# Optimization experiments

Hardware: AMD Instinct MI355X
Metric: run time of the kernel (lower is better)

## Reference

```python
import jax, jax.numpy as jnp
import numpy as np

CH = 512      # channels
CI = CH // 4  # in_channel = 128
DILS = (1, 4, 8, 12)
GN_GROUPS = 32


def conv2d(x, w, dil=1, pad=0):
    # x: (N,Cin,H,W), w: (Cout,Cin,kh,kw)
    return jax.lax.conv_general_dilated(
        x, w, window_strides=(1, 1), padding=[(pad, pad), (pad, pad)],
        rhs_dilation=(dil, dil),
        dimension_numbers=('NCHW', 'OIHW', 'NCHW'))


def group_norm(x, gamma, beta, groups=GN_GROUPS, eps=1e-5):
    N, C, H, W = x.shape
    xg = x.reshape(N, groups, C // groups, H, W)
    mu = jnp.mean(xg, axis=(2, 3, 4), keepdims=True)
    var = jnp.var(xg, axis=(2, 3, 4), keepdims=True)
    xn = ((xg - mu) * jax.lax.rsqrt(var + eps)).reshape(N, C, H, W)
    return xn * gamma[None, :, None, None] + beta[None, :, None, None]


def dyn_branch(xd, w_cat, d):
    # dynamic filter: (N, 9, H, W), softmax over the K=9 taps per pixel
    f = jax.nn.softmax(conv2d(xd, w_cat, dil=d, pad=d), axis=1)
    N, C, H, W = xd.shape
    xp = jnp.pad(xd, ((0, 0), (0, 0), (d, d), (d, d)))
    # fused unfold + weighted sum: accumulate 9 shifted views * per-pixel weight
    out = jnp.zeros_like(xd)
    k = 0
    for i in range(3):
        for j in range(3):
            out = out + xp[:, :, i * d:i * d + H, j * d:j * d + W] * f[:, k:k + 1]
            k += 1
    return out


def setup_inputs():
    key = jax.random.key(0)
    ks = jax.random.split(key, 16)
    s = 0.05
    return {
        'x': jax.random.normal(ks[0], (4, CH, 128, 128), jnp.float32),
        'w_scale1': jax.random.normal(ks[1], (CI, CH, 1, 1), jnp.float32) * s,
        'gn1_g': jnp.ones((CI,), jnp.float32),
        'gn1_b': jnp.zeros((CI,), jnp.float32),
        'w_cata': jax.random.normal(ks[2], (9, CI, 3, 3), jnp.float32) * s,
        'w_catb': jax.random.normal(ks[3], (9, CI, 3, 3), jnp.float32) * s,
        'w_catc': jax.random.normal(ks[4], (9, CI, 3, 3), jnp.float32) * s,
        'w_catd': jax.random.normal(ks[5], (9, CI, 3, 3), jnp.float32) * s,
        'w_scale2': jax.random.normal(ks[6], (CI, 5 * CI, 1, 1), jnp.float32) * s,
        'gn2_g': jnp.ones((CI,), jnp.float32),
        'gn2_b': jnp.zeros((CI,), jnp.float32),
        'w_scale3': jax.random.normal(ks[7], (CH, CI, 1, 1), jnp.float32) * s,
        'gn3_g': jnp.ones((CH,), jnp.float32),
        'gn3_b': jnp.zeros((CH,), jnp.float32),
    }


def reference(x, w_scale1, gn1_g, gn1_b, w_cata, w_catb, w_catc, w_catd,
              w_scale2, gn2_g, gn2_b, w_scale3, gn3_g, gn3_b):
    # scale1: 1x1 conv -> GN -> ReLU
    xd = jax.nn.relu(group_norm(conv2d(x, w_scale1), gn1_g, gn1_b))
    # four dilated dynamic-filter branches (unfold + softmax-weighted reduce)
    outs = [dyn_branch(xd, w, d)
            for w, d in zip((w_cata, w_catb, w_catc, w_catd), DILS)]
    cat = jnp.concatenate([xd] + outs, axis=1)  # (N, 5*CI, H, W)
    y = jax.nn.relu(group_norm(conv2d(cat, w_scale2), gn2_g, gn2_b))
    y = jax.nn.relu(group_norm(conv2d(y, w_scale3), gn3_g, gn3_b))
    return y
```

## Files before the change

kernel.cpp:

```cpp
#include <hip/hip_runtime.h>
#include <math.h>

#define HW 16384

typedef float f32x4 __attribute__((ext_vector_type(4)));
typedef __bf16 bf16x8 __attribute__((ext_vector_type(8)));
typedef unsigned short u16x4 __attribute__((ext_vector_type(4)));
typedef unsigned short u16x8 __attribute__((ext_vector_type(8)));

__device__ __forceinline__ unsigned short f2bf(float f) {
  unsigned u = __float_as_uint(f);
  u += 0x7fffu + ((u >> 16) & 1u);
  return (unsigned short)(u >> 16);
}
__device__ __forceinline__ float bf2f(unsigned short s) {
  return __uint_as_float(((unsigned)s) << 16);
}

__global__ void prep_kernel(const float* __restrict__ w1, const float* __restrict__ w2,
                            const float* __restrict__ w3,
                            const float* __restrict__ wa, const float* __restrict__ wb,
                            const float* __restrict__ wc, const float* __restrict__ wd,
                            unsigned short* __restrict__ w1b, unsigned short* __restrict__ w2b,
                            unsigned short* __restrict__ w3b, unsigned short* __restrict__ wr) {
  int idx = blockIdx.x * 256 + threadIdx.x;
  if (idx < 65536) { w1b[idx] = f2bf(w1[idx]); }
  else if (idx < 147456) { int j = idx - 65536; w2b[j] = f2bf(w2[j]); }
  else if (idx < 212992) { int j = idx - 147456; w3b[j] = f2bf(w3[j]); }
  else if (idx < 286720) {
    int j = idx - 212992;
    int br = j / 18432, rem = j % 18432;
    int tap = rem / 2048, rem2 = rem % 2048;
    int kt = rem2 / 128, c = rem2 % 128;
    const float* w = (br == 0) ? wa : (br == 1) ? wb : (br == 2) ? wc : wd;
    float v = (kt < 9) ? w[(kt * 128 + c) * 9 + tap] : 0.f;
    wr[j] = f2bf(v);
  }
}

__device__ __forceinline__ void gn_partial_epilogue(
    f32x4 (&acc)[8], int wv, int lane, int t, int n, int blkx,
    float* __restrict__ part, float (*ps)[32], float (*pss)[32]) {
  float gs[8], gss[8];
#pragma unroll
  for (int cb = 0; cb < 8; ++cb) {
    float s = 0.f, ss = 0.f;
#pragma unroll
    for (int r = 0; r < 4; ++r) { float v = acc[cb][r]; s += v; ss += v * v; }
#pragma unroll
    for (int m = 0; m < 4; ++m) {
      const int msk[4] = {1, 2, 16, 32};
      s += __shfl_xor(s, msk[m]); ss += __shfl_xor(ss, msk[m]);
    }
    gs[cb] = s; gss[cb] = ss;
  }
  if (lane < 16 && (lane & 3) == 0) {
    int q = lane >> 2;
#pragma unroll
    for (int cb = 0; cb < 8; ++cb) { ps[wv][cb * 4 + q] = gs[cb]; pss[wv][cb * 4 + q] = gss[cb]; }
  }
  __syncthreads();
  if (t < 32) {
    float a = ps[0][t] + ps[1][t] + ps[2][t] + ps[3][t];
    float b = pss[0][t] + pss[1][t] + pss[2][t] + pss[3][t];
    float* pp = part + ((size_t)(n * 32 + t) * 256 + blkx) * 2;
    pp[0] = a; pp[1] = b;
  }
}

__global__ __launch_bounds__(256) void conv1f_kernel(
    const float* __restrict__ x, const unsigned short* __restrict__ w1b,
    unsigned short* __restrict__ outb, float* __restrict__ part) {
  __shared__ float xs[2][64][65];
  __shared__ float ps[4][32], pss[4][32];
  int t = threadIdx.x;
  int wv = t >> 6, lane = t & 63, lr = lane & 15, lg = lane >> 4;
  int n = blockIdx.y;
  int p0 = blockIdx.x * 64;
  const float* xn = x + (size_t)n * 512 * HW + p0;
  f32x4 acc[8];
#pragma unroll
  for (int cb = 0; cb < 8; ++cb) acc[cb] = (f32x4){0.f, 0.f, 0.f, 0.f};

  int ci_l = t >> 4, px4 = (t & 15) * 4;
  float4 r[4];

#pragma unroll
  for (int pass = 0; pass < 4; ++pass)
    r[pass] = *(const float4*)(xn + (size_t)(pass * 16 + ci_l) * HW + px4);
#pragma unroll
  for (int pass = 0; pass < 4; ++pass) {
    int cl = pass * 16 + ci_l;
    xs[0][cl][px4 + 0] = r[pass].x; xs[0][cl][px4 + 1] = r[pass].y;
    xs[0][cl][px4 + 2] = r[pass].z; xs[0][cl][px4 + 3] = r[pass].w;
  }

  for (int kt = 0; kt < 8; ++kt) {
    int cur = kt & 1;
    if (kt < 7) {
#pragma unroll
      for (int pass = 0; pass < 4; ++pass)
        r[pass] = *(const float4*)(xn + (size_t)((kt + 1) * 64 + pass * 16 + ci_l) * HW + px4);
    }
    __syncthreads();
#pragma unroll
    for (int ks = 0; ks < 2; ++ks) {
      bf16x8 a;
#pragma unroll
      for (int j = 0; j < 8; ++j) {
        unsigned short us = f2bf(xs[cur][ks * 32 + lg * 8 + j][wv * 16 + lr]);
        a[j] = *(__bf16*)&us;
      }
#pragma unroll
      for (int cb = 0; cb < 8; ++cb) {
        bf16x8 b = *(const bf16x8*)(w1b + (size_t)(cb * 16 + lr) * 512
                                    + kt * 64 + ks * 32 + lg * 8);
        acc[cb] = __builtin_amdgcn_mfma_f32_16x16x32_bf16(a, b, acc[cb], 0, 0, 0);
      }
    }
    if (kt < 7) {
#pragma unroll
      for (int pass = 0; pass < 4; ++pass) {
        int cl = pass * 16 + ci_l;
        xs[cur ^ 1][cl][px4 + 0] = r[pass].x; xs[cur ^ 1][cl][px4 + 1] = r[pass].y;
        xs[cur ^ 1][cl][px4 + 2] = r[pass].z; xs[cur ^ 1][cl][px4 + 3] = r[pass].w;
      }
    }
  }
  unsigned short* on = outb + (size_t)n * HW * 640;
#pragma unroll
  for (int cb = 0; cb < 8; ++cb)
#pragma unroll
    for (int r2 = 0; r2 < 4; ++r2)
      on[(size_t)(p0 + wv * 16 + lg * 4 + r2) * 640 + cb * 16 + lr] = f2bf(acc[cb][r2]);
  __syncthreads();
  gn_partial_epilogue(acc, wv, lane, t, n, blockIdx.x, part, ps, pss);
}

template<int K>
__global__ __launch_bounds__(256) void conv_pm_kernel(
    const unsigned short* __restrict__ act, const unsigned short* __restrict__ w,
    unsigned short* __restrict__ outb, float* __restrict__ part, int ldd) {
  __shared__ float ps[4][32], pss[4][32];
  int t = threadIdx.x;
  int wv = t >> 6, lane = t & 63;
  int lr = lane & 15, lg = lane >> 4;
  int n = blockIdx.y;
  int p0 = blockIdx.x * 64 + wv * 16;
  const unsigned short* an = act + (size_t)n * HW * K;
  f32x4 acc[8];
#pragma unroll
  for (int cb = 0; cb < 8; ++cb) acc[cb] = (f32x4){0.f, 0.f, 0.f, 0.f};
  const unsigned short* ap = an + (size_t)(p0 + lr) * K + lg * 8;
  const unsigned short* bp = w + (size_t)lr * K + lg * 8;
  constexpr int NK = K / 32;

  bf16x8 a_c, b_c[8], a_n, b_n[8];
  a_c = *(const bf16x8*)(ap);
#pragma unroll
  for (int cb = 0; cb < 8; ++cb) b_c[cb] = *(const bf16x8*)(bp + (size_t)cb * 16 * K);

#pragma unroll
  for (int ks = 0; ks < NK; ++ks) {
    if (ks + 1 < NK) {
      a_n = *(const bf16x8*)(ap + (ks + 1) * 32);
#pragma unroll
      for (int cb = 0; cb < 8; ++cb)
        b_n[cb] = *(const bf16x8*)(bp + (size_t)cb * 16 * K + (ks + 1) * 32);
    }
#pragma unroll
    for (int cb = 0; cb < 8; ++cb)
      acc[cb] = __builtin_amdgcn_mfma_f32_16x16x32_bf16(a_c, b_c[cb], acc[cb], 0, 0, 0);
    if (ks + 1 < NK) {
      a_c = a_n;
#pragma unroll
      for (int cb = 0; cb < 8; ++cb) b_c[cb] = b_n[cb];
    }
  }
  unsigned short* on = outb + (size_t)n * HW * ldd;
#pragma unroll
  for (int cb = 0; cb < 8; ++cb)
#pragma unroll
    for (int r = 0; r < 4; ++r)
      on[(size_t)(p0 + lg * 4 + r) * ldd + cb * 16 + lr] = f2bf(acc[cb][r]);
  gn_partial_epilogue(acc, wv, lane, t, n, blockIdx.x, part, ps, pss);
}

__global__ __launch_bounds__(1024) void gnf256_kernel(
    const float* __restrict__ part, float* __restrict__ stats) {
  __shared__ float sh[1024], sh2[1024];
  int t = threadIdx.x;
  int tg = t >> 3, sub = t & 7;
  float s = 0.f, ss = 0.f;
  for (int b = sub * 32; b < sub * 32 + 32; ++b) {
    const float* pp = part + ((size_t)tg * 256 + b) * 2;
    s += pp[0]; ss += pp[1];
  }
  sh[t] = s; sh2[t] = ss;
  __syncthreads();
  if (t < 128) {
    float a = 0.f, b2 = 0.f;
#pragma unroll
    for (int i = 0; i < 8; ++i) { a += sh[t * 8 + i]; b2 += sh2[t * 8 + i]; }
    float inv = 1.f / (4.f * HW);
    float mean = a * inv, var = b2 * inv - mean * mean;
    stats[2 * t] = mean; stats[2 * t + 1] = rsqrtf(var + 1e-5f);
  }
}

__global__ __launch_bounds__(256) void gna_ip_kernel(
    unsigned short* __restrict__ dst, const float* __restrict__ stats,
    const float* __restrict__ gamma, const float* __restrict__ beta, int ldd) {
  int idx = blockIdx.x * 256 + threadIdx.x;
  int g = idx & 31;
  int p = (idx >> 5) & (HW - 1);
  int n = idx >> 19;
  unsigned short* ptr = dst + ((size_t)n * HW + p) * ldd + 4 * g;
  u16x4 v = *(u16x4*)ptr;
  int sg = n * 32 + g;
  float mean = stats[2 * sg], rstd = stats[2 * sg + 1];
  float sc0 = rstd * gamma[4 * g + 0], sc1 = rstd * gamma[4 * g + 1];
  float sc2 = rstd * gamma[4 * g + 2], sc3 = rstd * gamma[4 * g + 3];
  float sh0 = beta[4 * g + 0] - mean * sc0, sh1 = beta[4 * g + 1] - mean * sc1;
  float sh2 = beta[4 * g + 2] - mean * sc2, sh3 = beta[4 * g + 3] - mean * sc3;
  u16x4 o;
  o[0] = f2bf(fmaxf(fmaf(bf2f(v[0]), sc0, sh0), 0.f));
  o[1] = f2bf(fmaxf(fmaf(bf2f(v[1]), sc1, sh1), 0.f));
  o[2] = f2bf(fmaxf(fmaf(bf2f(v[2]), sc2, sh2), 0.f));
  o[3] = f2bf(fmaxf(fmaf(bf2f(v[3]), sc3, sh3), 0.f));
  *(u16x4*)ptr = o;
}

__global__ __launch_bounds__(256) void conv3_kernel(
    const unsigned short* __restrict__ y, const unsigned short* __restrict__ w3,
    unsigned short* __restrict__ outb, float* __restrict__ part) {
  int wv = threadIdx.x >> 6, lane = threadIdx.x & 63;
  int lr = lane & 15, lg = lane >> 4;
  int n = blockIdx.y, zc = blockIdx.z;
  int co0 = zc * 128 + wv * 32;
  int p0 = blockIdx.x * 128;
  const unsigned short* yn = y + (size_t)n * HW * 128;
  f32x4 acc[2][8];
#pragma unroll
  for (int pr = 0; pr < 2; ++pr)
#pragma unroll
    for (int cb = 0; cb < 8; ++cb) acc[pr][cb] = (f32x4){0.f, 0.f, 0.f, 0.f};
#pragma unroll
  for (int ks = 0; ks < 4; ++ks) {
    bf16x8 a0 = *(const bf16x8*)(w3 + (size_t)(co0 + lr) * 128 + ks * 32 + lg * 8);
    bf16x8 a1 = *(const bf16x8*)(w3 + (size_t)(co0 + 16 + lr) * 128 + ks * 32 + lg * 8);
#pragma unroll
    for (int cb = 0; cb < 8; ++cb) {
      bf16x8 b = *(const bf16x8*)(yn + (size_t)(p0 + cb * 16 + lr) * 128 + ks * 32 + lg * 8);
      acc[0][cb] = __builtin_amdgcn_mfma_f32_16x16x32_bf16(a0, b, acc[0][cb], 0, 0, 0);
      acc[1][cb] = __builtin_amdgcn_mfma_f32_16x16x32_bf16(a1, b, acc[1][cb], 0, 0, 0);
    }
  }
  unsigned short* on = outb + (size_t)n * 512 * HW;
  float s[2] = {0.f, 0.f}, ss[2] = {0.f, 0.f};
#pragma unroll
  for (int pr = 0; pr < 2; ++pr)
#pragma unroll
    for (int cb = 0; cb < 8; ++cb)
#pragma unroll
      for (int r = 0; r < 4; ++r) {
        float v = acc[pr][cb][r];
        on[(size_t)(co0 + pr * 16 + lg * 4 + r) * HW + p0 + cb * 16 + lr] = f2bf(v);
        s[pr] += v; ss[pr] += v * v;
      }
#pragma unroll
  for (int pr = 0; pr < 2; ++pr) {
    float a = s[pr], b = ss[pr];
    for (int m = 1; m < 64; m <<= 1) { a += __shfl_xor(a, m); b += __shfl_xor(b, m); }
    if (lane == 0) {
      float* pp = part + ((((size_t)n * 4 + zc) * 128 + blockIdx.x) * 8 + wv * 2 + pr) * 2;
      pp[0] = a; pp[1] = b;
    }
  }
}

__global__ __launch_bounds__(1024) void gnf3_kernel(
    const float* __restrict__ part, float* __restrict__ stats) {
  __shared__ float sh[1024], sh2[1024];
  int t = threadIdx.x;
  int e = t >> 3, xbs = t & 7;
  int n = e >> 5, g = e & 31;
  int zc = g >> 3, sub = g & 7;
  float s = 0.f, ss = 0.f;
  for (int xb = xbs * 16; xb < xbs * 16 + 16; ++xb) {
    const float* pp = part + ((((size_t)n * 4 + zc) * 128 + xb) * 8 + sub) * 2;
    s += pp[0]; ss += pp[1];
  }
  sh[t] = s; sh2[t] = ss;
  __syncthreads();
  if (t < 128) {
    float a = 0.f, b2 = 0.f;
#pragma unroll
    for (int i = 0; i < 8; ++i) { a += sh[t * 8 + i]; b2 += sh2[t * 8 + i]; }
    float inv = 1.f / (16.f * HW);
    float mean = a * inv, var = b2 * inv - mean * mean;
    stats[2 * t] = mean; stats[2 * t + 1] = rsqrtf(var + 1e-5f);
  }
}

__global__ __launch_bounds__(256) void gn3_apply_kernel(
    const unsigned short* __restrict__ y3b, const float* __restrict__ stats,
    const float* __restrict__ gamma, const float* __restrict__ beta,
    float* __restrict__ out) {
  size_t e8 = ((size_t)blockIdx.x * 256 + threadIdx.x) * 8;
  int n = (int)(e8 >> 23);
  int c = (int)((e8 >> 14) & 511);
  int sg = n * 32 + (c >> 4);
  float mean = stats[2 * sg], rstd = stats[2 * sg + 1];
  float scale = rstd * gamma[c];
  float shift = beta[c] - mean * scale;
  u16x8 u = *(const u16x8*)(y3b + e8);
  float4 o0, o1;
  o0.x = fmaxf(fmaf(bf2f(u[0]), scale, shift), 0.f);
  o0.y = fmaxf(fmaf(bf2f(u[1]), scale, shift), 0.f);
  o0.z = fmaxf(fmaf(bf2f(u[2]), scale, shift), 0.f);
  o0.w = fmaxf(fmaf(bf2f(u[3]), scale, shift), 0.f);
  o1.x = fmaxf(fmaf(bf2f(u[4]), scale, shift), 0.f);
  o1.y = fmaxf(fmaf(bf2f(u[5]), scale, shift), 0.f);
  o1.z = fmaxf(fmaf(bf2f(u[6]), scale, shift), 0.f);
  o1.w = fmaxf(fmaf(bf2f(u[7]), scale, shift), 0.f);
  *(float4*)(out + e8) = o0;
  *(float4*)(out + e8 + 4) = o1;
}

#define DP 136
#define DSLOTS 56

__global__ __launch_bounds__(512, 6) void dynfused8_kernel(
    const unsigned short* __restrict__ cat, const unsigned short* __restrict__ wr,
    unsigned short* __restrict__ catw) {
  extern __shared__ char smem[];
  unsigned short* rowbuf = (unsigned short*)smem;
  float* fl = (float*)(smem + 3 * DSLOTS * DP * 2);
  int t = threadIdx.x;
  int bid = blockIdx.x;
  int rh = ((bid & 7) << 6) + (bid >> 3);
  int row = rh >> 2, qw = rh & 3;
  int n = blockIdx.y >> 2, br = blockIdx.y & 3;
  int d = (br == 0) ? 1 : 4 * br;
  const unsigned short* xb = cat + (size_t)n * HW * 640;

  int rg[3] = { max(row - d, 0), row, min(row + d, 127) };
  bool rv[3] = { row - d >= 0, true, row + d < 128 };
  int cbase = qw * 32 - 12;

  {
    u16x8 vreg[6];
#pragma unroll
    for (int k = 0; k < 6; ++k) {
      int ci = t + (k << 9);
      if (k == 5 && ci >= 2688) continue;
      int s = (ci >= 1792) ? 2 : (ci >= 896 ? 1 : 0);
      int rem = ci - s * 896;
      int slot = rem >> 4, c = rem & 15;
      int gcol = min(max(cbase + slot, 0), 127);
      vreg[k] = *(const u16x8*)(xb + ((size_t)(rg[s] * 128 + gcol)) * 640 + c * 8);
    }
#pragma unroll
    for (int k = 0; k < 6; ++k) {
      int ci = t + (k << 9);
      if (k == 5 && ci >= 2688) continue;
      int s = (ci >= 1792) ? 2 : (ci >= 896 ? 1 : 0);
      int rem = ci - s * 896;
      int slot = rem >> 4, c = rem & 15;
      *(u16x8*)(rowbuf + ((size_t)s * DSLOTS + slot) * DP + c * 8) = vreg[k];
    }
  }
  __syncthreads();

  if (t < 128) {
    int wv = t >> 6, lane = t & 63;
    int lr = lane & 15, lg = lane >> 4;
    const unsigned short* wb = wr + (size_t)br * 9 * 16 * 128;
    const bf16x8 zb = {(__bf16)0.f, (__bf16)0.f, (__bf16)0.f, (__bf16)0.f,
                       (__bf16)0.f, (__bf16)0.f, (__bf16)0.f, (__bf16)0.f};
    f32x4 acc = (f32x4){0.f, 0.f, 0.f, 0.f};
    int pxl = wv * 16 + lr;
    int gw = qw * 32 + pxl;
#pragma unroll
    for (int tap = 0; tap < 9; ++tap) {
      int s = tap / 3;
      int dw = (tap % 3 - 1) * d;
      int slot = 12 + pxl + dw;
      bool val = rv[s] && ((unsigned)(gw + dw) < 128u);
      const unsigned short* ap = rowbuf + ((size_t)s * DSLOTS + slot) * DP + lg * 8;
      const unsigned short* wt = wb + (size_t)(tap * 16 + lr) * 128 + lg * 8;
#pragma unroll
      for (int ks = 0; ks < 4; ++ks) {
        bf16x8 a = *(const bf16x8*)(ap + ks * 32);
        if (!val) a = zb;
        bf16x8 b = *(const bf16x8*)(wt + ks * 32);
        acc = __builtin_amdgcn_mfma_f32_16x16x32_bf16(a, b, acc, 0, 0, 0);
      }
    }
#pragma unroll
    for (int r = 0; r < 4; ++r) {
      float v = acc[r];
      float m = (lr < 9) ? v : -3.0e38f;
#pragma unroll
      for (int msk = 1; msk < 16; msk <<= 1) m = fmaxf(m, __shfl_xor(m, msk));
      float e = (lr < 9) ? expf(v - m) : 0.f;
      float su = e;
#pragma unroll
      for (int msk = 1; msk < 16; msk <<= 1) su += __shfl_xor(su, msk);
      fl[(wv * 16 + lg * 4 + r) * 17 + lr] = e / su;
    }
  }
  __syncthreads();

  {
    int pxl = t >> 4, c16 = t & 15;
    int gw = qw * 32 + pxl;
    float oacc[8];
#pragma unroll
    for (int i = 0; i < 8; ++i) oacc[i] = 0.f;
#pragma unroll
    for (int tap = 0; tap < 9; ++tap) {
      int s = tap / 3;
      int dw = (tap % 3 - 1) * d;
      int slot = 12 + pxl + dw;
      bool val = rv[s] && ((unsigned)(gw + dw) < 128u);
      float f = val ? fl[pxl * 17 + tap] : 0.f;
      u16x8 u = *(const u16x8*)(rowbuf + ((size_t)s * DSLOTS + slot) * DP + c16 * 8);
#pragma unroll
      for (int i = 0; i < 8; ++i)
        oacc[i] = fmaf(f, bf2f(u[i]), oacc[i]);
    }
    unsigned short* orow = catw + ((size_t)n * HW + row * 128 + gw) * 640
                           + 128 * (br + 1) + c16 * 8;
    u16x8 o;
#pragma unroll
    for (int i = 0; i < 8; ++i) o[i] = f2bf(oacc[i]);
    *(u16x8*)orow = o;
  }
}

extern "C" void kernel_launch(void* const* d_in, const int* in_sizes, int n_in,
                              void* d_out, int out_size, void* d_ws, size_t ws_size,
                              hipStream_t stream) {
  const float* x   = (const float*)d_in[0];
  const float* w1  = (const float*)d_in[1];
  const float* g1  = (const float*)d_in[2];
  const float* b1  = (const float*)d_in[3];
  const float* wca = (const float*)d_in[4];
  const float* wcb = (const float*)d_in[5];
  const float* wcc = (const float*)d_in[6];
  const float* wcd = (const float*)d_in[7];
  const float* w2  = (const float*)d_in[8];
  const float* g2  = (const float*)d_in[9];
  const float* b2  = (const float*)d_in[10];
  const float* w3  = (const float*)d_in[11];
  const float* g3  = (const float*)d_in[12];
  const float* b3  = (const float*)d_in[13];
  float* out = (float*)d_out;

  float* ws = (float*)d_ws;
  unsigned short* cat = (unsigned short*)(ws + 25165824);
  unsigned short* y2b = (unsigned short*)(ws + 8388608);
  unsigned short* y3b = (unsigned short*)(ws + 25165824);
  float* aux = ws + 46137344;
  unsigned short* w1b = (unsigned short*)(aux);
  unsigned short* w2b = (unsigned short*)(aux + 32768);
  unsigned short* w3b = (unsigned short*)(aux + 73728);
  unsigned short* wr  = (unsigned short*)(aux + 106496);
  float* part  = aux + 143360;
  float* part3 = aux + 208896;
  float* st1   = aux + 241664;
  float* st2   = aux + 241920;
  float* st3   = aux + 242176;

  dim3 blk(256);
  const int dynLds = 3 * DSLOTS * DP * 2 + 32 * 17 * 4;
  (void)hipFuncSetAttribute((const void*)dynfused8_kernel,
                            hipFuncAttributeMaxDynamicSharedMemorySize, dynLds);

  prep_kernel<<<dim3(1120), blk, 0, stream>>>(w1, w2, w3, wca, wcb, wcc, wcd,
                                              w1b, w2b, w3b, wr);

  conv1f_kernel<<<dim3(256, 4), blk, 0, stream>>>(x, w1b, cat, part);
  gnf256_kernel<<<dim3(1), dim3(1024), 0, stream>>>(part, st1);
  gna_ip_kernel<<<dim3(8192), blk, 0, stream>>>(cat, st1, g1, b1, 640);

  dynfused8_kernel<<<dim3(512, 16), dim3(512), dynLds, stream>>>(cat, wr, cat);

  conv_pm_kernel<640><<<dim3(256, 4), blk, 0, stream>>>(cat, w2b, y2b, part, 128);
  gnf256_kernel<<<dim3(1), dim3(1024), 0, stream>>>(part, st2);
  gna_ip_kernel<<<dim3(8192), blk, 0, stream>>>(y2b, st2, g2, b2, 128);

  conv3_kernel<<<dim3(128, 4, 4), blk, 0, stream>>>(y2b, w3b, y3b, part3);
  gnf3_kernel<<<dim3(1), dim3(1024), 0, stream>>>(part3, st3);
  gn3_apply_kernel<<<dim3(16384), blk, 0, stream>>>(y3b, st3, g3, b3, out);
}
```

Before: 371.6 us.

## Compute GN3 stats algebraically via Gram matrix, fuse conv3 with normalize-apply

Instead of materializing the conv3 output in bf16 and re-reading it for group norm, the GN3 group sums and sums of squares are derived algebraically. They come from the 128x128 Gram matrix of y2 (per batch), column sums of y2, and precomputed per-group weight products W^T W. conv3 is then recomputed with normalization and ReLU fused into its epilogue, writing fp32 output directly. This removes the 64 MB bf16 intermediate write/read and a separate apply pass, but adds Gram-matrix MFMA work, a 64-way partial reduction through a large scratch buffer, and several small kernels. The stats also now come from bf16-rounded weights through a different summation order.

```diff
diff --git a/kernel.cpp b/kernel.cpp
--- a/kernel.cpp
+++ b/kernel.cpp
@@ -35,6 +35,32 @@
     const float* w = (br == 0) ? wa : (br == 1) ? wb : (br == 2) ? wc : wd;
     float v = (kt < 9) ? w[(kt * 128 + c) * 9 + tap] : 0.f;
     wr[j] = f2bf(v);
+  }
+}
+
+__global__ __launch_bounds__(256) void prepM_kernel(
+    const unsigned short* __restrict__ w3b, float* __restrict__ M,
+    float* __restrict__ wsumg) {
+  __shared__ float wl[16][128];
+  int g = blockIdx.x, t = threadIdx.x;
+#pragma unroll
+  for (int k = 0; k < 8; ++k) {
+    int e = t + k * 256;
+    wl[e >> 7][e & 127] = bf2f(w3b[(size_t)(g * 16 + (e >> 7)) * 128 + (e & 127)]);
+  }
+  __syncthreads();
+  for (int e = t; e < 16384; e += 256) {
+    int i = e >> 7, j = e & 127;
+    float s = 0.f;
+#pragma unroll
+    for (int r = 0; r < 16; ++r) s += wl[r][i] * wl[r][j];
+    M[(size_t)g * 16384 + e] = s;
+  }
+  if (t < 128) {
+    float s = 0.f;
+#pragma unroll
+    for (int r = 0; r < 16; ++r) s += wl[r][t];
+    wsumg[g * 128 + t] = s;
   }
 }
 
@@ -231,9 +257,132 @@
   *(u16x4*)ptr = o;
 }
 
-__global__ __launch_bounds__(256) void conv3_kernel(
+__global__ __launch_bounds__(256) void colsum_kernel(
+    const unsigned short* __restrict__ y, float* __restrict__ csp) {
+  __shared__ float sh[16][128];
+  int sl = blockIdx.x, n = blockIdx.y, t = threadIdx.x;
+  int c16 = t & 15, ph = t >> 4;
+  const unsigned short* yn = y + (size_t)n * HW * 128;
+  float a[8] = {0.f, 0.f, 0.f, 0.f, 0.f, 0.f, 0.f, 0.f};
+  for (int p = sl * 1024 + ph; p < (sl + 1) * 1024; p += 16) {
+    u16x8 u = *(const u16x8*)(yn + (size_t)p * 128 + c16 * 8);
+#pragma unroll
+    for (int j = 0; j < 8; ++j) a[j] += bf2f(u[j]);
+  }
+#pragma unroll
+  for (int j = 0; j < 8; ++j) sh[ph][c16 * 8 + j] = a[j];
+  __syncthreads();
+  if (t < 128) {
+    float s = 0.f;
+#pragma unroll
+    for (int p2 = 0; p2 < 16; ++p2) s += sh[p2][t];
+    csp[(size_t)(n * 16 + sl) * 128 + t] = s;
+  }
+}
+
+__global__ __launch_bounds__(256) void smat_kernel(
+    const unsigned short* __restrict__ y, float* __restrict__ spart) {
+  __shared__ unsigned short ych[128][136];
+  int t = threadIdx.x;
+  int kc = blockIdx.x, n = blockIdx.y;
+  int wv = t >> 6, lane = t & 63, lr = lane & 15, lg = lane >> 4;
+  const unsigned short* yn = y + (size_t)n * HW * 128;
+  int p0 = kc * 256;
+  f32x4 acc[2][8];
+#pragma unroll
+  for (int i2 = 0; i2 < 2; ++i2)
+#pragma unroll
+    for (int jt = 0; jt < 8; ++jt) acc[i2][jt] = (f32x4){0.f, 0.f, 0.f, 0.f};
+
+  for (int s2 = 0; s2 < 2; ++s2) {
+    __syncthreads();
+#pragma unroll
+    for (int k = 0; k < 8; ++k) {
+      int idx = t + (k << 8);
+      int p = idx >> 4, c8 = idx & 15;
+      u16x8 u = *(const u16x8*)(yn + (size_t)(p0 + s2 * 128 + p) * 128 + c8 * 8);
+#pragma unroll
+      for (int j = 0; j < 8; ++j) ych[c8 * 8 + j][p] = u[j];
+    }
+    __syncthreads();
+#pragma unroll
+    for (int ks = 0; ks < 4; ++ks) {
+      bf16x8 a[2], b[8];
+      a[0] = *(const bf16x8*)&ych[(wv * 2 + 0) * 16 + lr][ks * 32 + lg * 8];
+      a[1] = *(const bf16x8*)&ych[(wv * 2 + 1) * 16 + lr][ks * 32 + lg * 8];
+#pragma unroll
+      for (int jt = 0; jt < 8; ++jt)
+        b[jt] = *(const bf16x8*)&ych[jt * 16 + lr][ks * 32 + lg * 8];
+#pragma unroll
+      for (int i2 = 0; i2 < 2; ++i2)
+#pragma unroll
+        for (int jt = 0; jt < 8; ++jt)
+          acc[i2][jt] = __builtin_amdgcn_mfma_f32_16x16x32_bf16(a[i2], b[jt], acc[i2][jt], 0, 0, 0);
+    }
+  }
+  float* sp = spart + (size_t)(n * 64 + kc) * 16384;
+#pragma unroll
+  for (int i2 = 0; i2 < 2; ++i2)
+#pragma unroll
+    for (int jt = 0; jt < 8; ++jt)
+#pragma unroll
+      for (int r = 0; r < 4; ++r)
+        sp[(size_t)((wv * 2 + i2) * 16 + lg * 4 + r) * 128 + jt * 16 + lr] = acc[i2][jt][r];
+}
+
+__global__ __launch_bounds__(256) void reduceS_kernel(
+    const float* __restrict__ spart, float* __restrict__ sfull) {
+  int e = blockIdx.x * 256 + threadIdx.x;
+  int n = e >> 14, ij = e & 16383;
+  float s = 0.f;
+  for (int kc = 0; kc < 64; ++kc)
+    s += spart[((size_t)(n * 64 + kc) << 14) + ij];
+  sfull[e] = s;
+}
+
+__global__ __launch_bounds__(256) void stats3_kernel(
+    const float* __restrict__ M, const float* __restrict__ sfull,
+    const float* __restrict__ wsumg, const float* __restrict__ csp,
+    float* __restrict__ stats) {
+  __shared__ float sh[256];
+  int bid = blockIdx.x;
+  int n = bid >> 5, g = bid & 31;
+  int t = threadIdx.x;
+  float ss = 0.f;
+  for (int e = t; e < 16384; e += 256)
+    ss += M[(size_t)g * 16384 + e] * sfull[(size_t)n * 16384 + e];
+  sh[t] = ss; __syncthreads();
+  for (int st = 128; st > 0; st >>= 1) {
+    if (t < st) sh[t] += sh[t + st];
+    __syncthreads();
+  }
+  float sstot = sh[0];
+  __syncthreads();
+  float cm = 0.f;
+  if (t < 128) {
+    float cs = 0.f;
+#pragma unroll
+    for (int sl = 0; sl < 16; ++sl) cs += csp[(size_t)(n * 16 + sl) * 128 + t];
+    cm = wsumg[g * 128 + t] * cs;
+  }
+  sh[t] = (t < 128) ? cm : 0.f; __syncthreads();
+  for (int st = 128; st > 0; st >>= 1) {
+    if (t < st) sh[t] += sh[t + st];
+    __syncthreads();
+  }
+  if (t == 0) {
+    float inv = 1.f / (16.f * HW);
+    float mean = sh[0] * inv;
+    float var = sstot * inv - mean * mean;
+    stats[2 * bid] = mean;
+    stats[2 * bid + 1] = rsqrtf(var + 1e-5f);
+  }
+}
+
+__global__ __launch_bounds__(256) void conv3_apply_kernel(
     const unsigned short* __restrict__ y, const unsigned short* __restrict__ w3,
-    unsigned short* __restrict__ outb, float* __restrict__ part) {
+    const float* __restrict__ stats, const float* __restrict__ gamma,
+    const float* __restrict__ beta, float* __restrict__ out) {
   int wv = threadIdx.x >> 6, lane = threadIdx.x & 63;
   int lr = lane & 15, lg = lane >> 4;
   int n = blockIdx.y, zc = blockIdx.z;
@@ -256,76 +405,24 @@
       acc[1][cb] = __builtin_amdgcn_mfma_f32_16x16x32_bf16(a1, b, acc[1][cb], 0, 0, 0);
     }
   }
-  unsigned short* on = outb + (size_t)n * 512 * HW;
-  float s[2] = {0.f, 0.f}, ss[2] = {0.f, 0.f};
-#pragma unroll
-  for (int pr = 0; pr < 2; ++pr)
-#pragma unroll
-    for (int cb = 0; cb < 8; ++cb)
-#pragma unroll
-      for (int r = 0; r < 4; ++r) {
-        float v = acc[pr][cb][r];
-        on[(size_t)(co0 + pr * 16 + lg * 4 + r) * HW + p0 + cb * 16 + lr] = f2bf(v);
-        s[pr] += v; ss[pr] += v * v;
+  float* on = out + (size_t)n * 512 * HW;
+#pragma unroll
+  for (int pr = 0; pr < 2; ++pr) {
+    int gbase = zc * 8 + wv * 2 + pr;
+    int sg = n * 32 + gbase;
+    float mean = stats[2 * sg], rstd = stats[2 * sg + 1];
+#pragma unroll
+    for (int r = 0; r < 4; ++r) {
+      int co = co0 + pr * 16 + lg * 4 + r;
+      float sc = rstd * gamma[co];
+      float sh = beta[co] - mean * sc;
+#pragma unroll
+      for (int cb = 0; cb < 8; ++cb) {
+        float v = fmaxf(fmaf(acc[pr][cb][r], sc, sh), 0.f);
+        on[(size_t)co * HW + p0 + cb * 16 + lr] = v;
       }
-#pragma unroll
-  for (int pr = 0; pr < 2; ++pr) {
-    float a = s[pr], b = ss[pr];
-    for (int m = 1; m < 64; m <<= 1) { a += __shfl_xor(a, m); b += __shfl_xor(b, m); }
-    if (lane == 0) {
-      float* pp = part + ((((size_t)n * 4 + zc) * 128 + blockIdx.x) * 8 + wv * 2 + pr) * 2;
-      pp[0] = a; pp[1] = b;
-    }
-  }
-}
-
-__global__ __launch_bounds__(1024) void gnf3_kernel(
-    const float* __restrict__ part, float* __restrict__ stats) {
-  __shared__ float sh[1024], sh2[1024];
-  int t = threadIdx.x;
-  int e = t >> 3, xbs = t & 7;
-  int n = e >> 5, g = e & 31;
-  int zc = g >> 3, sub = g & 7;
-  float s = 0.f, ss = 0.f;
-  for (int xb = xbs * 16; xb < xbs * 16 + 16; ++xb) {
-    const float* pp = part + ((((size_t)n * 4 + zc) * 128 + xb) * 8 + sub) * 2;
-    s += pp[0]; ss += pp[1];
-  }
-  sh[t] = s; sh2[t] = ss;
-  __syncthreads();
-  if (t < 128) {
-    float a = 0.f, b2 = 0.f;
-#pragma unroll
-    for (int i = 0; i < 8; ++i) { a += sh[t * 8 + i]; b2 += sh2[t * 8 + i]; }
-    float inv = 1.f / (16.f * HW);
-    float mean = a * inv, var = b2 * inv - mean * mean;
-    stats[2 * t] = mean; stats[2 * t + 1] = rsqrtf(var + 1e-5f);
-  }
-}
-
-__global__ __launch_bounds__(256) void gn3_apply_kernel(
-    const unsigned short* __restrict__ y3b, const float* __restrict__ stats,
-    const float* __restrict__ gamma, const float* __restrict__ beta,
-    float* __restrict__ out) {
-  size_t e8 = ((size_t)blockIdx.x * 256 + threadIdx.x) * 8;
-  int n = (int)(e8 >> 23);
-  int c = (int)((e8 >> 14) & 511);
-  int sg = n * 32 + (c >> 4);
-  float mean = stats[2 * sg], rstd = stats[2 * sg + 1];
-  float scale = rstd * gamma[c];
-  float shift = beta[c] - mean * scale;
-  u16x8 u = *(const u16x8*)(y3b + e8);
-  float4 o0, o1;
-  o0.x = fmaxf(fmaf(bf2f(u[0]), scale, shift), 0.f);
-  o0.y = fmaxf(fmaf(bf2f(u[1]), scale, shift), 0.f);
-  o0.z = fmaxf(fmaf(bf2f(u[2]), scale, shift), 0.f);
-  o0.w = fmaxf(fmaf(bf2f(u[3]), scale, shift), 0.f);
-  o1.x = fmaxf(fmaf(bf2f(u[4]), scale, shift), 0.f);
-  o1.y = fmaxf(fmaf(bf2f(u[5]), scale, shift), 0.f);
-  o1.z = fmaxf(fmaf(bf2f(u[6]), scale, shift), 0.f);
-  o1.w = fmaxf(fmaf(bf2f(u[7]), scale, shift), 0.f);
-  *(float4*)(out + e8) = o0;
-  *(float4*)(out + e8 + 4) = o1;
+    }
+  }
 }
 
 #define DP 136
@@ -460,19 +557,22 @@
   float* out = (float*)d_out;
 
   float* ws = (float*)d_ws;
+  float* spart = ws;
   unsigned short* cat = (unsigned short*)(ws + 25165824);
   unsigned short* y2b = (unsigned short*)(ws + 8388608);
-  unsigned short* y3b = (unsigned short*)(ws + 25165824);
   float* aux = ws + 46137344;
   unsigned short* w1b = (unsigned short*)(aux);
   unsigned short* w2b = (unsigned short*)(aux + 32768);
   unsigned short* w3b = (unsigned short*)(aux + 73728);
   unsigned short* wr  = (unsigned short*)(aux + 106496);
-  float* part  = aux + 143360;
-  float* part3 = aux + 208896;
-  float* st1   = aux + 241664;
-  float* st2   = aux + 241920;
-  float* st3   = aux + 242176;
+  float* part   = aux + 143360;
+  float* Mbuf   = aux + 208896;
+  float* wsumg  = aux + 733184;
+  float* sfull  = aux + 737280;
+  float* csp    = aux + 802816;
+  float* st1    = aux + 811008;
+  float* st2    = aux + 811264;
+  float* st3    = aux + 811520;
 
   dim3 blk(256);
   const int dynLds = 3 * DSLOTS * DP * 2 + 32 * 17 * 4;
@@ -481,6 +581,7 @@
 
   prep_kernel<<<dim3(1120), blk, 0, stream>>>(w1, w2, w3, wca, wcb, wcc, wcd,
                                               w1b, w2b, w3b, wr);
+  prepM_kernel<<<dim3(32), blk, 0, stream>>>(w3b, Mbuf, wsumg);
 
   conv1f_kernel<<<dim3(256, 4), blk, 0, stream>>>(x, w1b, cat, part);
   gnf256_kernel<<<dim3(1), dim3(1024), 0, stream>>>(part, st1);
@@ -492,7 +593,9 @@
   gnf256_kernel<<<dim3(1), dim3(1024), 0, stream>>>(part, st2);
   gna_ip_kernel<<<dim3(8192), blk, 0, stream>>>(y2b, st2, g2, b2, 128);
 
-  conv3_kernel<<<dim3(128, 4, 4), blk, 0, stream>>>(y2b, w3b, y3b, part3);
-  gnf3_kernel<<<dim3(1), dim3(1024), 0, stream>>>(part3, st3);
-  gn3_apply_kernel<<<dim3(16384), blk, 0, stream>>>(y3b, st3, g3, b3, out);
-}
+  colsum_kernel<<<dim3(16, 4), blk, 0, stream>>>(y2b, csp);
+  smat_kernel<<<dim3(64, 4), blk, 0, stream>>>(y2b, spart);
+  reduceS_kernel<<<dim3(256), blk, 0, stream>>>(spart, sfull);
+  stats3_kernel<<<dim3(128), blk, 0, stream>>>(Mbuf, sfull, wsumg, csp, st3);
+  conv3_apply_kernel<<<dim3(128, 4, 4), blk, 0, stream>>>(y2b, w3b, st3, g3, b3, out);
+}
```

New measurement: 410.0 us. 1.1x slower.
